# Kernel optimization log

Hardware: AMD Instinct MI355X
Metric: run time of the kernel (lower is better)

## Reference

```python
import jax, jax.numpy as jnp
import numpy as np

B, CIN, COUT, T, K = 8, 64, 64, 16384, 127


def setup_inputs() -> dict:
    key = jax.random.key(0)
    kx, kw = jax.random.split(key)
    x = jax.random.normal(kx, (B, CIN, T), dtype=jnp.float32)
    sigma = np.sqrt(2.0 / (CIN * K + COUT)).astype(np.float32)
    W = jax.random.normal(kw, (COUT, CIN, K), dtype=jnp.float32) * sigma
    return {"x": x, "W": W}


def reference(x, W):
    # Full linear convolution via FFT (true convolution, matches
    # torchaudio.functional.fftconvolve), summed over in_channels,
    # then trimmed to mode='same' (output length == T, centered).
    T_ = x.shape[-1]
    K_ = W.shape[-1]
    n = T_ + K_ - 1  # linear-conv length, no circular wraparound
    Xf = jnp.fft.rfft(x, n=n)   # [B, Cin, nf] complex
    Wf = jnp.fft.rfft(W, n=n)   # [Cout, Cin, nf] complex
    # Batched complex multiply-accumulate over in_channels (single pass,
    # no per-output-channel redundant FFTs).
    Yf = jnp.einsum('bif,oif->bof', Xf, Wf)  # [B, Cout, nf]
    y_full = jnp.fft.irfft(Yf, n=n)          # [B, Cout, T+K-1]
    start = (K_ - 1) // 2                    # 'same': centered crop
    return y_full[..., start:start + T_]
```

## Files before the change

kernel.cpp:

```cpp
#include <hip/hip_runtime.h>

#define T_LEN 16384
#define CIN   64
#define COUT  64
#define KTAPS 127
#define TN    512
#define XROWS 640
#define WT_KS 4096

typedef __attribute__((ext_vector_type(8)))  __bf16 bf16x8;
typedef __attribute__((ext_vector_type(16))) float  f32x16;
typedef __attribute__((ext_vector_type(4)))  float  float4v;

__device__ inline unsigned short f2bf(float f) {
    unsigned u = __builtin_bit_cast(unsigned, f);
    u += 0x7fffu + ((u >> 16) & 1u);
    return (unsigned short)(u >> 16);
}

__global__ void wt_transform(const float* __restrict__ W,
                             unsigned short* __restrict__ Wt) {
    int t  = blockIdx.x * 256 + threadIdx.x;
    int kp = t >> 9, c = t & 511;
    int f = c >> 6, kg = (c >> 5) & 1, l31 = c & 31;
    int cc = f >> 1, m = f & 1;
    int o = m * 32 + l31, ib = cc * 16 + kg * 8;
    const float* src = W + (o * CIN + ib) * KTAPS + (126 - kp);
    unsigned short tmp[8];
    #pragma unroll
    for (int e = 0; e < 8; ++e)
        tmp[e] = f2bf(src[e * KTAPS]);
    uint4 pk;
    pk.x = (unsigned)tmp[0] | ((unsigned)tmp[1] << 16);
    pk.y = (unsigned)tmp[2] | ((unsigned)tmp[3] << 16);
    pk.z = (unsigned)tmp[4] | ((unsigned)tmp[5] << 16);
    pk.w = (unsigned)tmp[6] | ((unsigned)tmp[7] << 16);
    *(uint4*)(Wt + kp * WT_KS + c * 8) = pk;
}

__global__ __launch_bounds__(512, 2)
void conv_mfma(const float* __restrict__ x,
               const unsigned short* __restrict__ Wt,
               float* __restrict__ y) {
    __shared__ __align__(16) char pool[81920];
    unsigned short* xs = (unsigned short*)pool;

    const int tid = threadIdx.x;
    const int bb  = blockIdx.x >> 5;
    const int tt  = blockIdx.x & 31;
    const int t0  = tt * TN;

    {
        const int cin = tid >> 3;
        const int s   = tid & 7;
        const float* xrow = x + (bb * CIN + cin) * T_LEN;
        const int p = cin >> 2, c3 = cin & 3;
        for (int j = 0; j < 20; ++j) {
            const int w = 32 * j + 4 * s;
            const int u = t0 - 64 + w;
            float4v v;
            if (u >= 0 && u + 4 <= T_LEN) {
                v = *(const float4v*)(xrow + u);
            } else {
                v.x = (u + 0 >= 0 && u + 0 < T_LEN) ? xrow[u + 0] : 0.f;
                v.y = (u + 1 >= 0 && u + 1 < T_LEN) ? xrow[u + 1] : 0.f;
                v.z = (u + 2 >= 0 && u + 2 < T_LEN) ? xrow[u + 2] : 0.f;
                v.w = (u + 3 >= 0 && u + 3 < T_LEN) ? xrow[u + 3] : 0.f;
            }
            #pragma unroll
            for (int e = 0; e < 4; ++e) {
                const int we = w + e;
                const float fv = (e == 0) ? v.x : (e == 1) ? v.y : (e == 2) ? v.z : v.w;
                xs[we * 64 + ((p ^ (we & 15)) << 2) + c3] = f2bf(fv);
            }
        }
    }

    const int lane   = tid & 63;
    const int wv     = tid >> 6;
    const int quad   = wv >> 2;
    const int ww     = wv & 3;
    const int l31    = lane & 31;
    const int kg     = lane >> 5;
    const int twbase = ww * 128;
    const int brow0  = twbase + l31 + 1;

    const int kp0  = quad ? 64 : 0;
    const int ntap = quad ? 63 : 64;

    const char* ab = (const char*)Wt + lane * 16;

    f32x16 acc[2][4] = {};
    uint4 a0r[8], a1r[8];
    uint2 bAlo[4], bAhi[4];
    uint2 bBlo[4], bBhi[4];

    #define LOADA(dst, kp)                                                  \
        do { const char* p_ = ab + (kp) * 8192;                             \
            _Pragma("unroll")                                               \
            for (int f = 0; f < 8; ++f)                                     \
                dst[f] = *(const uint4*)(p_ + f * 1024); } while (0)

    #define LOADB(lo, hi, rb, cidx)                                         \
        do { const int rb15_ = (rb) & 15;                                   \
            const char* xp_ = (const char*)xs + (rb) * 128;                 \
            const int q0_ = (((4 * (cidx) + 2 * kg + 0) ^ rb15_) << 3);     \
            const int q1_ = (((4 * (cidx) + 2 * kg + 1) ^ rb15_) << 3);     \
            _Pragma("unroll")                                               \
            for (int n = 0; n < 4; ++n) {                                   \
                lo[n] = *(const uint2*)(xp_ + n * 4096 + q0_);              \
                hi[n] = *(const uint2*)(xp_ + n * 4096 + q1_);              \
            } } while (0)

    #define MFMAB(lo, hi, ar, cidx)                                         \
        do { bf16x8 a0 = __builtin_bit_cast(bf16x8, ar[(cidx) * 2 + 0]);    \
            bf16x8 a1 = __builtin_bit_cast(bf16x8, ar[(cidx) * 2 + 1]);     \
            _Pragma("unroll")                                               \
            for (int n = 0; n < 4; ++n) {                                   \
                uint4 t4 = {lo[n].x, lo[n].y, hi[n].x, hi[n].y};            \
                bf16x8 b = __builtin_bit_cast(bf16x8, t4);                  \
                acc[0][n] = __builtin_amdgcn_mfma_f32_32x32x16_bf16(a0, b, acc[0][n], 0, 0, 0); \
                acc[1][n] = __builtin_amdgcn_mfma_f32_32x32x16_bf16(a1, b, acc[1][n], 0, 0, 0); \
            } } while (0)

    #define TAP(ar, kp)                                                     \
        do {                                                                \
            LOADB(bBlo, bBhi, brow0 + (kp), 1);  MFMAB(bAlo, bAhi, ar, 0);  \
            LOADB(bAlo, bAhi, brow0 + (kp), 2);  MFMAB(bBlo, bBhi, ar, 1);  \
            LOADB(bBlo, bBhi, brow0 + (kp), 3);  MFMAB(bAlo, bAhi, ar, 2);  \
            LOADB(bAlo, bAhi, brow0 + (kp) + 1, 0); MFMAB(bBlo, bBhi, ar, 3); \
        } while (0)

    LOADA(a0r, kp0);
    __syncthreads();
    LOADB(bAlo, bAhi, brow0 + kp0, 0);

    for (int i = 0; i < ntap; i += 2) {
        if (i + 1 < ntap) LOADA(a1r, kp0 + i + 1);
        TAP(a0r, kp0 + i);
        if (i + 2 < ntap) LOADA(a0r, kp0 + i + 2);
        if (i + 1 < ntap) TAP(a1r, kp0 + i + 1);
    }

    __syncthreads();
    float* msm = (float*)pool;
    #pragma unroll
    for (int m = 0; m < 2; ++m) {
        if (quad == 1) {
            #pragma unroll
            for (int n = 0; n < 4; ++n)
                #pragma unroll
                for (int r = 0; r < 16; ++r)
                    msm[(n * 16 + r) * 256 + ww * 64 + lane] = acc[m][n][r];
        }
        __syncthreads();
        if (quad == 0) {
            #pragma unroll
            for (int n = 0; n < 4; ++n)
                #pragma unroll
                for (int r = 0; r < 16; ++r)
                    acc[m][n][r] += msm[(n * 16 + r) * 256 + ww * 64 + lane];
        }
        __syncthreads();
    }

    if (quad == 0) {
        const int ybase = (bb * COUT) * T_LEN;
        #pragma unroll
        for (int m = 0; m < 2; ++m) {
            #pragma unroll
            for (int n = 0; n < 4; ++n) {
                const int t = t0 + twbase + n * 32 + l31;
                #pragma unroll
                for (int r = 0; r < 16; ++r) {
                    const int o = m * 32 + (r & 3) + 8 * (r >> 2) + 4 * kg;
                    y[ybase + o * T_LEN + t] = acc[m][n][r];
                }
            }
        }
    }
}

extern "C" void kernel_launch(void* const* d_in, const int* in_sizes, int n_in,
                              void* d_out, int out_size, void* d_ws, size_t ws_size,
                              hipStream_t stream) {
    const float* x = (const float*)d_in[0];
    const float* W = (const float*)d_in[1];
    float* yout = (float*)d_out;
    unsigned short* Wt = (unsigned short*)d_ws;

    wt_transform<<<(KTAPS * 512) / 256, 256, 0, stream>>>(W, Wt);

    const int grid = 8 * (T_LEN / TN);
    conv_mfma<<<grid, 512, 0, stream>>>(x, Wt, yout);
}
```

Before: 119.7 us.

## Use padded LDS pitch for x tile enabling 128-bit B-fragment reads

Replaces the XOR-swizzled 128-byte-row LDS layout for the x tile with a padded 144-byte row pitch, so each B fragment becomes one contiguous 16-byte LDS read instead of two 8-byte reads plus register shuffling. It also raises wave priority around the MFMA bursts with s_setprio. The padding is meant to avoid bank conflicts on the wide reads, but the store pattern during staging may now conflict, and the LDS footprint grows slightly (92160 bytes vs 81920).

```diff
diff --git a/kernel.cpp b/kernel.cpp
--- a/kernel.cpp
+++ b/kernel.cpp
@@ -6,6 +6,7 @@
 #define KTAPS 127
 #define TN    512
 #define XROWS 640
+#define XPITCH_B 144
 #define WT_KS 4096
 
 typedef __attribute__((ext_vector_type(8)))  __bf16 bf16x8;
@@ -42,7 +43,7 @@
 void conv_mfma(const float* __restrict__ x,
                const unsigned short* __restrict__ Wt,
                float* __restrict__ y) {
-    __shared__ __align__(16) char pool[81920];
+    __shared__ __align__(16) char pool[XROWS * XPITCH_B];
     unsigned short* xs = (unsigned short*)pool;
 
     const int tid = threadIdx.x;
@@ -54,7 +55,6 @@
         const int cin = tid >> 3;
         const int s   = tid & 7;
         const float* xrow = x + (bb * CIN + cin) * T_LEN;
-        const int p = cin >> 2, c3 = cin & 3;
         for (int j = 0; j < 20; ++j) {
             const int w = 32 * j + 4 * s;
             const int u = t0 - 64 + w;
@@ -71,7 +71,7 @@
             for (int e = 0; e < 4; ++e) {
                 const int we = w + e;
                 const float fv = (e == 0) ? v.x : (e == 1) ? v.y : (e == 2) ? v.z : v.w;
-                xs[we * 64 + ((p ^ (we & 15)) << 2) + c3] = f2bf(fv);
+                xs[we * 72 + cin] = f2bf(fv);
             }
         }
     }
@@ -92,8 +92,7 @@
 
     f32x16 acc[2][4] = {};
     uint4 a0r[8], a1r[8];
-    uint2 bAlo[4], bAhi[4];
-    uint2 bBlo[4], bBhi[4];
+    uint4 bA[4], bB[4];
 
     #define LOADA(dst, kp)                                                  \
         do { const char* p_ = ab + (kp) * 8192;                             \
@@ -101,39 +100,37 @@
             for (int f = 0; f < 8; ++f)                                     \
                 dst[f] = *(const uint4*)(p_ + f * 1024); } while (0)
 
-    #define LOADB(lo, hi, rb, cidx)                                         \
-        do { const int rb15_ = (rb) & 15;                                   \
-            const char* xp_ = (const char*)xs + (rb) * 128;                 \
-            const int q0_ = (((4 * (cidx) + 2 * kg + 0) ^ rb15_) << 3);     \
-            const int q1_ = (((4 * (cidx) + 2 * kg + 1) ^ rb15_) << 3);     \
+    #define LOADB(dst, rb, cidx)                                            \
+        do { const char* xp_ = (const char*)xs + (rb) * XPITCH_B            \
+                               + ((2 * (cidx) + kg) << 4);                  \
+            _Pragma("unroll")                                               \
+            for (int n = 0; n < 4; ++n)                                     \
+                dst[n] = *(const uint4*)(xp_ + n * (32 * XPITCH_B));        \
+        } while (0)
+
+    #define MFMAB(bv, ar, cidx)                                             \
+        do { bf16x8 a0 = __builtin_bit_cast(bf16x8, ar[(cidx) * 2 + 0]);    \
+            bf16x8 a1 = __builtin_bit_cast(bf16x8, ar[(cidx) * 2 + 1]);     \
+            __builtin_amdgcn_s_setprio(1);                                  \
             _Pragma("unroll")                                               \
             for (int n = 0; n < 4; ++n) {                                   \
-                lo[n] = *(const uint2*)(xp_ + n * 4096 + q0_);              \
-                hi[n] = *(const uint2*)(xp_ + n * 4096 + q1_);              \
-            } } while (0)
-
-    #define MFMAB(lo, hi, ar, cidx)                                         \
-        do { bf16x8 a0 = __builtin_bit_cast(bf16x8, ar[(cidx) * 2 + 0]);    \
-            bf16x8 a1 = __builtin_bit_cast(bf16x8, ar[(cidx) * 2 + 1]);     \
-            _Pragma("unroll")                                               \
-            for (int n = 0; n < 4; ++n) {                                   \
-                uint4 t4 = {lo[n].x, lo[n].y, hi[n].x, hi[n].y};            \
-                bf16x8 b = __builtin_bit_cast(bf16x8, t4);                  \
+                bf16x8 b = __builtin_bit_cast(bf16x8, bv[n]);               \
                 acc[0][n] = __builtin_amdgcn_mfma_f32_32x32x16_bf16(a0, b, acc[0][n], 0, 0, 0); \
                 acc[1][n] = __builtin_amdgcn_mfma_f32_32x32x16_bf16(a1, b, acc[1][n], 0, 0, 0); \
-            } } while (0)
+            }                                                               \
+            __builtin_amdgcn_s_setprio(0); } while (0)
 
     #define TAP(ar, kp)                                                     \
         do {                                                                \
-            LOADB(bBlo, bBhi, brow0 + (kp), 1);  MFMAB(bAlo, bAhi, ar, 0);  \
-            LOADB(bAlo, bAhi, brow0 + (kp), 2);  MFMAB(bBlo, bBhi, ar, 1);  \
-            LOADB(bBlo, bBhi, brow0 + (kp), 3);  MFMAB(bAlo, bAhi, ar, 2);  \
-            LOADB(bAlo, bAhi, brow0 + (kp) + 1, 0); MFMAB(bBlo, bBhi, ar, 3); \
+            LOADB(bB, brow0 + (kp), 1);     MFMAB(bA, ar, 0);               \
+            LOADB(bA, brow0 + (kp), 2);     MFMAB(bB, ar, 1);               \
+            LOADB(bB, brow0 + (kp), 3);     MFMAB(bA, ar, 2);               \
+            LOADB(bA, brow0 + (kp) + 1, 0); MFMAB(bB, ar, 3);               \
         } while (0)
 
     LOADA(a0r, kp0);
     __syncthreads();
-    LOADB(bAlo, bAhi, brow0 + kp0, 0);
+    LOADB(bA, brow0 + kp0, 0);
 
     for (int i = 0; i < ntap; i += 2) {
         if (i + 1 < ntap) LOADA(a1r, kp0 + i + 1);
```

Measured after the change: 118.2 us. Within noise of the previous version (-1.3%).
